# Kernel tuning notes

Hardware: AMD Instinct MI355X
Metric: run time of the kernel (lower is better)

The kernel has to match this reference:

```python
import jax, jax.numpy as jnp
import numpy as np

B, N, C = 8, 1024, 1024
H = 16
D = C // H  # head_dim = 64
SCALE = D ** -0.5


def setup_inputs() -> dict:
    key = jax.random.key(0)
    k1, k2, k3, k4 = jax.random.split(key, 4)
    x = jax.random.normal(k1, (B, N, C), dtype=jnp.float32)
    qkv_w = jax.random.normal(k2, (3 * C, C), dtype=jnp.float32) * (C ** -0.5)
    proj_w = jax.random.normal(k3, (C, C), dtype=jnp.float32) * (C ** -0.5)
    proj_b = jax.random.normal(k4, (C,), dtype=jnp.float32)
    return {"x": x, "qkv_w": qkv_w, "proj_w": proj_w, "proj_b": proj_b}


def reference(x, qkv_w, proj_w, proj_b):
    # qkv projection: torch Linear weight is [out, in] -> x @ W^T
    qkv = jnp.einsum('bnc,oc->bno', x, qkv_w)            # [B, N, 3C]
    qkv = qkv.reshape(B, N, 3, H, D)
    q = jnp.transpose(qkv[:, :, 0], (0, 2, 1, 3))        # [B, H, N, D]
    k = jnp.transpose(qkv[:, :, 1], (0, 2, 1, 3))
    v = jnp.transpose(qkv[:, :, 2], (0, 2, 1, 3))
    attn = jnp.einsum('bhqd,bhkd->bhqk', q, k) * SCALE   # [B, H, N, N]
    attn = jax.nn.softmax(attn, axis=-1)
    out = jnp.einsum('bhqk,bhkd->bhqd', attn, v)         # [B, H, N, D]
    out = jnp.transpose(out, (0, 2, 1, 3)).reshape(B, N, C)
    out = jnp.einsum('bnc,oc->bno', out, proj_w) + proj_b
    return out
```

## Files before the change

kernel.cpp:

```cpp
#include <hip/hip_runtime.h>
#include <hip/hip_bf16.h>
#include <stdint.h>

#define B_ 8
#define N_ 1024
#define C_ 1024
#define H_ 16

static constexpr float SCALE = 0.125f;
static constexpr float LOG2E = 1.4426950408889634f;
static constexpr float SL    = SCALE * LOG2E;

typedef __attribute__((ext_vector_type(4))) float f32x4;
typedef __attribute__((ext_vector_type(8))) short s16x8;

__device__ __forceinline__ ushort f2bf(float f) {
    union { float f; uint32_t u; } c; c.f = f;
    uint32_t u = c.u;
    return (ushort)((u + 0x7fffu + ((u >> 16) & 1u)) >> 16);
}

__device__ __forceinline__ ushort f2bfc(float f) {
    union { __hip_bfloat16 h; ushort u; } c;
    c.h = __float2bfloat16(f);
    return c.u;
}

__device__ __forceinline__ void gload_lds16(const void* g, void* l) {
    __builtin_amdgcn_global_load_lds(
        (const __attribute__((address_space(1))) void*)g,
        (__attribute__((address_space(3))) void*)l,
        16, 0, 0);
}
__device__ __forceinline__ void gload_lds4(const void* g, void* l) {
    __builtin_amdgcn_global_load_lds(
        (const __attribute__((address_space(1))) void*)g,
        (__attribute__((address_space(3))) void*)l,
        4, 0, 0);
}

__global__ __launch_bounds__(256) void cvt_f32_bf16(const float* __restrict__ in,
                                                    ushort* __restrict__ out, int n4) {
    int i = blockIdx.x * 256 + threadIdx.x;
    if (i >= n4) return;
    float4 v = ((const float4*)in)[i];
    ushort4 o = make_ushort4(f2bf(v.x), f2bf(v.y), f2bf(v.z), f2bf(v.w));
    ((ushort4*)out)[i] = o;
}

template<int OUT_BF16>
__global__ __launch_bounds__(256) void gemm_bt(const ushort* __restrict__ A,
                                               const ushort* __restrict__ Bw,
                                               void* __restrict__ Cout,
                                               const float* __restrict__ bias,
                                               int M, int Nout, int K) {
    __shared__ ushort Asm[128 * 64];
    __shared__ ushort Bsm[128 * 64];
    const int t = threadIdx.x;
    const int l = t & 63, w = t >> 6;
    const int lq = l & 15, lg = l >> 4;
    const int trow = blockIdx.y * 128, tcol = blockIdx.x * 128;
    const int wrow = (w >> 1) * 64, wcol = (w & 1) * 64;

    f32x4 acc[4][4] = {};

    const int srow0 = t >> 3;
    const int sc8 = (((t & 7) ^ (srow0 & 7)) * 8);
    const size_t abase = (size_t)(trow + srow0) * K + sc8;
    const size_t bbase = (size_t)(tcol + srow0) * K + sc8;

    for (int k0 = 0; k0 < K; k0 += 64) {
#pragma unroll
        for (int i = 0; i < 4; ++i) {
            gload_lds16(A + abase + (size_t)i * 32 * K + k0, &Asm[(i * 256 + w * 64) * 8]);
            gload_lds16(Bw + bbase + (size_t)i * 32 * K + k0, &Bsm[(i * 256 + w * 64) * 8]);
        }
        __syncthreads();
#pragma unroll
        for (int kk = 0; kk < 2; ++kk) {
            s16x8 af[4], bf[4];
#pragma unroll
            for (int m = 0; m < 4; ++m) {
                int row = wrow + m * 16 + lq;
                int ch = (kk * 4 + lg) ^ (row & 7);
                af[m] = *(const s16x8*)&Asm[row * 64 + ch * 8];
            }
#pragma unroll
            for (int n = 0; n < 4; ++n) {
                int row = wcol + n * 16 + lq;
                int ch = (kk * 4 + lg) ^ (row & 7);
                bf[n] = *(const s16x8*)&Bsm[row * 64 + ch * 8];
            }
#pragma unroll
            for (int m = 0; m < 4; ++m)
#pragma unroll
                for (int n = 0; n < 4; ++n)
                    acc[m][n] = __builtin_amdgcn_mfma_f32_16x16x32_bf16(af[m], bf[n], acc[m][n], 0, 0, 0);
        }
        __syncthreads();
    }

#pragma unroll
    for (int m = 0; m < 4; ++m)
#pragma unroll
        for (int n = 0; n < 4; ++n)
#pragma unroll
            for (int r = 0; r < 4; ++r) {
                int row = trow + wrow + m * 16 + lg * 4 + r;
                int col = tcol + wcol + n * 16 + lq;
                if (OUT_BF16) {
                    ((ushort*)Cout)[(size_t)row * Nout + col] = f2bfc(acc[m][n][r]);
                } else {
                    ((float*)Cout)[(size_t)row * Nout + col] = acc[m][n][r] + bias[col];
                }
            }
}

__global__ __launch_bounds__(256) void attn_fwd(const ushort* __restrict__ qk,
                                                const ushort* __restrict__ vt,
                                                ushort* __restrict__ attn_out) {
    __shared__ ushort Klds[64 * 64];
    __shared__ ushort Vlds[64 * 64];

    const int t = threadIdx.x, l = t & 63, w = t >> 6;
    const int lq = l & 15, lg = l >> 4;

    const int serial = blockIdx.x + 16 * blockIdx.y;
    const int logical = (serial & 7) * 256 + (serial >> 3);
    const int qt = logical & 15;
    const int bh = logical >> 4;
    const int b = bh >> 4, h = bh & 15;

    const int qrow = qt * 64 + w * 16 + lq;
    const size_t qoff = (size_t)(b * N_ + qrow) * 2048 + h * 64;
    const s16x8 qf0 = *(const s16x8*)&qk[qoff + lg * 8];
    const s16x8 qf1 = *(const s16x8*)&qk[qoff + 32 + lg * 8];

    float l_run = 0.f;
    f32x4 o[4] = {};

    const int srow0 = t >> 3;
    const int sc8 = ((t & 7) ^ (srow0 & 7)) * 8;
    const size_t kgbase = (size_t)(b * N_ + srow0) * 2048 + 1024 + h * 64 + sc8;

    const ushort* vptr[8];
#pragma unroll
    for (int j = 0; j < 8; ++j) {
        const int d = 16 * w + 2 * j + (l >> 5);
        const int c = ((l & 31) >> 2) ^ (d & 7);
        const int s = c * 8 + (l & 3) * 2;
        const int key = (s >> 5) * 32 + ((s >> 2) & 1) * 16 + ((s >> 3) & 3) * 4 + (s & 3);
        vptr[j] = vt + (size_t)(h * 64 + d) * (B_ * N_) + b * N_ + key;
    }

    for (int kt = 0; kt < N_ / 64; ++kt) {
        const size_t koff = kgbase + (size_t)kt * 64 * 2048;
        gload_lds16(qk + koff, &Klds[w * 512]);
        gload_lds16(qk + koff + (size_t)32 * 2048, &Klds[2048 + w * 512]);
#pragma unroll
        for (int j = 0; j < 8; ++j)
            gload_lds4(vptr[j] + kt * 64, &Vlds[w * 1024 + j * 128]);
        __syncthreads();

        f32x4 s[4];
#pragma unroll
        for (int g = 0; g < 4; ++g) {
            int key = g * 16 + lq;
            const s16x8 kf0 = *(const s16x8*)&Klds[key * 64 + ((lg ^ (key & 7)) * 8)];
            const s16x8 kf1 = *(const s16x8*)&Klds[key * 64 + (((4 + lg) ^ (key & 7)) * 8)];
            f32x4 z = {};
            z    = __builtin_amdgcn_mfma_f32_16x16x32_bf16(kf0, qf0, z, 0, 0, 0);
            s[g] = __builtin_amdgcn_mfma_f32_16x16x32_bf16(kf1, qf1, z, 0, 0, 0);
        }

        float pv[4][4];
        float psum = 0.f;
#pragma unroll
        for (int g = 0; g < 4; ++g) {
            float p0 = __builtin_amdgcn_exp2f(s[g][0] * SL);
            float p1 = __builtin_amdgcn_exp2f(s[g][1] * SL);
            float p2 = __builtin_amdgcn_exp2f(s[g][2] * SL);
            float p3 = __builtin_amdgcn_exp2f(s[g][3] * SL);
            psum += (p0 + p1) + (p2 + p3);
            pv[g][0] = p0; pv[g][1] = p1; pv[g][2] = p2; pv[g][3] = p3;
        }
        l_run += psum;

#pragma unroll
        for (int kb = 0; kb < 2; ++kb) {
            s16x8 pfrag;
#pragma unroll
            for (int i = 0; i < 4; ++i) {
                pfrag[i]     = (short)f2bfc(pv[2 * kb][i]);
                pfrag[4 + i] = (short)f2bfc(pv[2 * kb + 1][i]);
            }
#pragma unroll
            for (int ds = 0; ds < 4; ++ds) {
                const s16x8 vf = *(const s16x8*)
                    &Vlds[(ds * 16 + lq) * 64 + (((kb * 4 + lg) ^ (lq & 7)) * 8)];
                o[ds] = __builtin_amdgcn_mfma_f32_16x16x32_bf16(pfrag, vf, o[ds], 0, 0, 0);
            }
        }
        __syncthreads();
    }

    l_run += __shfl_xor(l_run, 16);
    l_run += __shfl_xor(l_run, 32);

#pragma unroll
    for (int r = 0; r < 4; ++r) {
        float rl = 1.f / __shfl(l_run, lg * 4 + r);
        int orow = qt * 64 + w * 16 + lg * 4 + r;
        size_t base = (size_t)(b * N_ + orow) * C_ + h * 64 + lq;
#pragma unroll
        for (int ds = 0; ds < 4; ++ds)
            attn_out[base + ds * 16] = f2bfc(o[ds][r] * rl);
    }
}

extern "C" void kernel_launch(void* const* d_in, const int* in_sizes, int n_in,
                              void* d_out, int out_size, void* d_ws, size_t ws_size,
                              hipStream_t stream) {
    const float* x      = (const float*)d_in[0];
    const float* qkv_w  = (const float*)d_in[1];
    const float* proj_w = (const float*)d_in[2];
    const float* proj_b = (const float*)d_in[3];
    float* out = (float*)d_out;

    ushort* ws    = (ushort*)d_ws;
    ushort* xb    = ws;
    ushort* wqkv  = xb + (size_t)8192 * 1024;
    ushort* wproj = wqkv + (size_t)3072 * 1024;
    ushort* qkb   = wproj + (size_t)1024 * 1024;
    ushort* vtb   = qkb + (size_t)8192 * 2048;
    ushort* attn  = vtb + (size_t)1024 * 8192;

    cvt_f32_bf16<<<8192, 256, 0, stream>>>(x, xb, 2097152);
    cvt_f32_bf16<<<3072, 256, 0, stream>>>(qkv_w, wqkv, 786432);
    cvt_f32_bf16<<<1024, 256, 0, stream>>>(proj_w, wproj, 262144);

    gemm_bt<1><<<dim3(16, 64), 256, 0, stream>>>(xb, wqkv, (void*)qkb, nullptr, 8192, 2048, 1024);
    gemm_bt<1><<<dim3(64, 8), 256, 0, stream>>>(wqkv + (size_t)2048 * 1024, xb, (void*)vtb,
                                                nullptr, 1024, 8192, 1024);

    attn_fwd<<<dim3(16, 128), 256, 0, stream>>>(qkb, vtb, attn);

    gemm_bt<0><<<dim3(8, 64), 256, 0, stream>>>(attn, wproj, (void*)out, proj_b, 8192, 1024, 1024);
}
```

Measured before the change: 173.0 us.

## Use 256x256 double-buffered GEMM for QK projection and fold softmax scale into Wq

Adds a new 512-thread GEMM kernel with 256x256 tiles, double-buffered LDS staging via global_load_lds, quadrant-wise MFMA scheduling with setprio, and XCD-aware block remapping. It replaces the 128x128 GEMM for the Q/K projection. Separately, the softmax scale times log2e is folded into the Q rows of the weight during bf16 conversion, which removes one multiply per score in attention. The bigger tile raises LDS and register use and leaves only 256 blocks, and rounding the scaled weight to bf16 changes numerics slightly.

```diff
diff --git a/kernel.cpp b/kernel.cpp
--- a/kernel.cpp
+++ b/kernel.cpp
@@ -45,6 +45,16 @@
     if (i >= n4) return;
     float4 v = ((const float4*)in)[i];
     ushort4 o = make_ushort4(f2bf(v.x), f2bf(v.y), f2bf(v.z), f2bf(v.w));
+    ((ushort4*)out)[i] = o;
+}
+
+__global__ __launch_bounds__(256) void cvt_qkvw(const float* __restrict__ in,
+                                                ushort* __restrict__ out, int n4) {
+    int i = blockIdx.x * 256 + threadIdx.x;
+    if (i >= n4) return;
+    float4 v = ((const float4*)in)[i];
+    const float sc = (i < (1024 * 1024 / 4)) ? SL : 1.0f;
+    ushort4 o = make_ushort4(f2bf(v.x * sc), f2bf(v.y * sc), f2bf(v.z * sc), f2bf(v.w * sc));
     ((ushort4*)out)[i] = o;
 }
 
@@ -116,6 +126,109 @@
             }
 }
 
+__global__ __launch_bounds__(512, 2) void gemm_bt256(const ushort* __restrict__ A,
+                                                     const ushort* __restrict__ Bw,
+                                                     ushort* __restrict__ Cout,
+                                                     int M, int Nout, int K) {
+    __shared__ ushort Asm[2][256 * 64];
+    __shared__ ushort Bsm[2][256 * 64];
+    const int t = threadIdx.x;
+    const int l = t & 63, w = t >> 6;
+    const int lq = l & 15, lg = l >> 4;
+    const int wm = w >> 2, wn = w & 3;
+
+    int bid = blockIdx.y * gridDim.x + blockIdx.x;
+    const int cpx = (gridDim.x * gridDim.y) >> 3;
+    bid = (bid & 7) * cpx + (bid >> 3);
+    const int bx = bid % gridDim.x, by = bid / gridDim.x;
+    const int trow = by * 256, tcol = bx * 256;
+
+    f32x4 acc[8][4] = {};
+
+    const int srow = t >> 3;
+    const int scc = ((t & 7) ^ (srow & 7)) * 8;
+    const size_t abase = (size_t)(trow + srow) * K + scc;
+    const size_t bbase = (size_t)(tcol + srow) * K + scc;
+
+#define STAGE256(buf, k0)                                                      \
+    {                                                                          \
+        _Pragma("unroll")                                                      \
+        for (int j = 0; j < 4; ++j) {                                          \
+            gload_lds16(A + abase + (size_t)j * 64 * K + (k0),                 \
+                        &Asm[buf][(j * 512 + t) * 8]);                         \
+            gload_lds16(Bw + bbase + (size_t)j * 64 * K + (k0),                \
+                        &Bsm[buf][(j * 512 + t) * 8]);                         \
+        }                                                                      \
+    }
+#define LOAD_A256(qr)                                                          \
+    _Pragma("unroll") for (int m = 0; m < 4; ++m) {                            \
+        const int row = wm * 128 + (qr) * 64 + m * 16 + lq;                    \
+        _Pragma("unroll") for (int kk = 0; kk < 2; ++kk)                       \
+            af[m][kk] = *(const s16x8*)&Asm[cur][row * 64 +                    \
+                            (((kk * 4 + lg) ^ (row & 7)) * 8)];                \
+    }
+#define LOAD_B256(qc)                                                          \
+    _Pragma("unroll") for (int n = 0; n < 2; ++n) {                            \
+        const int row = wn * 64 + (qc) * 32 + n * 16 + lq;                     \
+        _Pragma("unroll") for (int kk = 0; kk < 2; ++kk)                       \
+            bf[n][kk] = *(const s16x8*)&Bsm[cur][row * 64 +                    \
+                            (((kk * 4 + lg) ^ (row & 7)) * 8)];                \
+    }
+#define MFMA_Q256(qr, qc)                                                      \
+    __builtin_amdgcn_s_setprio(1);                                             \
+    _Pragma("unroll") for (int m = 0; m < 4; ++m)                              \
+        _Pragma("unroll") for (int n = 0; n < 2; ++n)                          \
+            _Pragma("unroll") for (int kk = 0; kk < 2; ++kk)                   \
+                acc[(qr) * 4 + m][(qc) * 2 + n] =                              \
+                    __builtin_amdgcn_mfma_f32_16x16x32_bf16(                   \
+                        af[m][kk], bf[n][kk], acc[(qr) * 4 + m][(qc) * 2 + n], \
+                        0, 0, 0);                                              \
+    __builtin_amdgcn_s_setprio(0);
+
+    STAGE256(0, 0);
+    asm volatile("s_waitcnt vmcnt(0)" ::: "memory");
+    __builtin_amdgcn_s_barrier();
+
+    const int NT = K / 64;
+    for (int kt = 0; kt < NT; ++kt) {
+        const int cur = kt & 1, nxt = cur ^ 1;
+        s16x8 af[4][2], bf[2][2];
+        LOAD_A256(0); LOAD_B256(0);
+        if (kt < NT - 1) STAGE256(nxt, (kt + 1) * 64);
+        __builtin_amdgcn_s_barrier();
+        MFMA_Q256(0, 0);
+        __builtin_amdgcn_s_barrier();
+        LOAD_B256(1);
+        __builtin_amdgcn_s_barrier();
+        MFMA_Q256(0, 1);
+        __builtin_amdgcn_s_barrier();
+        LOAD_A256(1);
+        __builtin_amdgcn_s_barrier();
+        MFMA_Q256(1, 1);
+        __builtin_amdgcn_s_barrier();
+        LOAD_B256(0);
+        __builtin_amdgcn_s_barrier();
+        MFMA_Q256(1, 0);
+        asm volatile("s_waitcnt vmcnt(0)" ::: "memory");
+        __builtin_amdgcn_s_barrier();
+    }
+
+#pragma unroll
+    for (int mt = 0; mt < 8; ++mt)
+#pragma unroll
+        for (int nt = 0; nt < 4; ++nt)
+#pragma unroll
+            for (int r = 0; r < 4; ++r) {
+                int row = trow + wm * 128 + mt * 16 + lg * 4 + r;
+                int col = tcol + wn * 64 + nt * 16 + lq;
+                Cout[(size_t)row * Nout + col] = f2bfc(acc[mt][nt][r]);
+            }
+#undef STAGE256
+#undef LOAD_A256
+#undef LOAD_B256
+#undef MFMA_Q256
+}
+
 __global__ __launch_bounds__(256) void attn_fwd(const ushort* __restrict__ qk,
                                                 const ushort* __restrict__ vt,
                                                 ushort* __restrict__ attn_out) {
@@ -177,10 +290,10 @@
         float psum = 0.f;
 #pragma unroll
         for (int g = 0; g < 4; ++g) {
-            float p0 = __builtin_amdgcn_exp2f(s[g][0] * SL);
-            float p1 = __builtin_amdgcn_exp2f(s[g][1] * SL);
-            float p2 = __builtin_amdgcn_exp2f(s[g][2] * SL);
-            float p3 = __builtin_amdgcn_exp2f(s[g][3] * SL);
+            float p0 = __builtin_amdgcn_exp2f(s[g][0]);
+            float p1 = __builtin_amdgcn_exp2f(s[g][1]);
+            float p2 = __builtin_amdgcn_exp2f(s[g][2]);
+            float p3 = __builtin_amdgcn_exp2f(s[g][3]);
             psum += (p0 + p1) + (p2 + p3);
             pv[g][0] = p0; pv[g][1] = p1; pv[g][2] = p2; pv[g][3] = p3;
         }
@@ -236,10 +349,10 @@
     ushort* attn  = vtb + (size_t)1024 * 8192;
 
     cvt_f32_bf16<<<8192, 256, 0, stream>>>(x, xb, 2097152);
-    cvt_f32_bf16<<<3072, 256, 0, stream>>>(qkv_w, wqkv, 786432);
+    cvt_qkvw<<<3072, 256, 0, stream>>>(qkv_w, wqkv, 786432);
     cvt_f32_bf16<<<1024, 256, 0, stream>>>(proj_w, wproj, 262144);
 
-    gemm_bt<1><<<dim3(16, 64), 256, 0, stream>>>(xb, wqkv, (void*)qkb, nullptr, 8192, 2048, 1024);
+    gemm_bt256<<<dim3(8, 32), 512, 0, stream>>>(xb, wqkv, qkb, 8192, 2048, 1024);
     gemm_bt<1><<<dim3(64, 8), 256, 0, stream>>>(wqkv + (size_t)2048 * 1024, xb, (void*)vtb,
                                                 nullptr, 1024, 8192, 1024);
 
```

Result: faster. 163.6 us (-5.4%).
